# Optimization experiments

Hardware: AMD Instinct MI355X
Metric: run time of the kernel (lower is better)

The kernel has to match this reference:

```python
import jax, jax.numpy as jnp
import numpy as np

L = 4          # num_layers
H = 512        # hidden_size == input_size
B, S = 8, 4096
LN_EPS = 1e-5


def parallel_scan_log(coeffs, values):
    """h_t = coeffs_t * h_{t-1} + values_t via Hillis-Steele log-step scan.
    coeffs, values: (B, S, H). Faithful to the torch loop incl. clamp."""
    seq_len = coeffs.shape[1]
    a = jnp.clip(coeffs, 1e-08, 1.0 - 1e-08)
    b = values
    num_steps = int(seq_len - 1).bit_length()
    for step in range(num_steps):
        d = 1 << step
        if d >= seq_len:
            break
        a_prev = jnp.pad(a[:, :-d, :], ((0, 0), (d, 0), (0, 0)), constant_values=1.0)
        b_prev = jnp.pad(b[:, :-d, :], ((0, 0), (d, 0), (0, 0)), constant_values=0.0)
        b = a * b_prev + b   # uses old a (matches a_new/b_new then assign)
        a = a * a_prev
    return b


def mingru_layer(x, Wz, bz, Wh, bh):
    # x: (B,S,in) ; Wz,Wh: (H,in) torch Linear layout (y = x @ W.T + b)
    z = jax.nn.sigmoid(jnp.einsum('bsi,hi->bsh', x, Wz) + bz)
    h_tilde = jnp.tanh(jnp.einsum('bsi,hi->bsh', x, Wh) + bh)
    return parallel_scan_log(1.0 - z, z * h_tilde)


def layer_norm(x, g, b):
    mu = jnp.mean(x, axis=-1, keepdims=True)
    var = jnp.mean(jnp.square(x - mu), axis=-1, keepdims=True)
    return (x - mu) * jax.lax.rsqrt(var + LN_EPS) * g + b


def run_layers(x, Wz, bz, Wh, bh, ln_g, ln_b):
    h = x
    for i in range(L):
        h_new = mingru_layer(h, Wz[i], bz[i], Wh[i], bh[i])
        if i > 0:
            h_new = h_new + h  # residual (shapes match for i>0)
        h = layer_norm(h_new, ln_g, ln_b)  # dropout==Identity (p=0)
    return h


def setup_inputs() -> dict:
    key = jax.random.key(0)
    ks = jax.random.split(key, 12)
    lim = 1.0 / np.sqrt(H)  # torch Linear default init range
    u = lambda k, shp: jax.random.uniform(k, shp, jnp.float32, -lim, lim)
    return {
        'x': jax.random.normal(ks[0], (B, S, H), jnp.float32),
        'Wz_f': u(ks[1], (L, H, H)), 'bz_f': u(ks[2], (L, H)),
        'Wh_f': u(ks[3], (L, H, H)), 'bh_f': u(ks[4], (L, H)),
        'Wz_b': u(ks[5], (L, H, H)), 'bz_b': u(ks[6], (L, H)),
        'Wh_b': u(ks[7], (L, H, H)), 'bh_b': u(ks[8], (L, H)),
        'fusion_w': u(ks[9], (H, 2 * H)), 'fusion_b': u(ks[10], (H,)),
        'ln_g': jnp.ones((H,), jnp.float32), 'ln_b': jnp.zeros((H,), jnp.float32),
    }


def reference(x, Wz_f, bz_f, Wh_f, bh_f, Wz_b, bz_b, Wh_b, bh_b, fusion_w, fusion_b, ln_g, ln_b):
    out_fwd = run_layers(x, Wz_f, bz_f, Wh_f, bh_f, ln_g, ln_b)
    x_rev = jnp.flip(x, axis=1)
    out_bwd = jnp.flip(run_layers(x_rev, Wz_b, bz_b, Wh_b, bh_b, ln_g, ln_b), axis=1)
    out_comb = jnp.concatenate([out_fwd, out_bwd], axis=-1)  # (B,S,2H)
    return jnp.einsum('bsk,hk->bsh', out_comb, fusion_w) + fusion_b
```

## Files before the change

kernel.cpp:

```cpp
#include <hip/hip_runtime.h>

#define HID 512
#define SLEN 4096
#define NB 8
#define BSROWS (NB*SLEN)
#define NLAYER 4
#define CHUNKT 128
#define NCHUNK 32

typedef float f32x4 __attribute__((ext_vector_type(4)));
typedef unsigned int u32x4 __attribute__((ext_vector_type(4)));

typedef const __attribute__((address_space(1))) unsigned int* gas_u32p;
typedef __attribute__((address_space(3))) unsigned int* las_u32p;

__device__ __forceinline__ float bf2f(unsigned short u){
  union { unsigned int i; float f; } v; v.i = ((unsigned int)u) << 16; return v.f;
}
__device__ __forceinline__ unsigned short f2bf(float f){
  union { float f; unsigned int i; } v; v.f = f;
  unsigned int u = v.i;
  u = u + 0x7fffu + ((u >> 16) & 1u);
  return (unsigned short)(u >> 16);
}
__device__ __forceinline__ void mfma_bf16(f32x4& acc, u32x4 a, u32x4 b){
  asm("v_mfma_f32_16x16x32_bf16 %0, %1, %2, %0" : "+v"(acc) : "v"(a), "v"(b));
}
__device__ __forceinline__ void mfma_fence(){
  __builtin_amdgcn_sched_barrier(0);
  asm volatile("s_nop 7\n\ts_nop 7\n\ts_nop 7\n\ts_nop 7");
  __builtin_amdgcn_sched_barrier(0);
}
__device__ __forceinline__ void decode_ab(unsigned int v, float& a, float& b){
  a = (float)(v & 0xffffu) * (1.f/65535.f);
  b = fmaf((float)(v >> 16), 2.f/65535.f, -1.f);
}
__device__ __forceinline__ void gload_lds16(const unsigned short* g, unsigned short* l){
  __builtin_amdgcn_global_load_lds((gas_u32p)(const void*)g, (las_u32p)(void*)l, 16, 0, 0);
}
__device__ __forceinline__ int scidx(int row, int col){
  return row*64 + (col ^ (((row>>2)&3)<<4));
}


__global__ __launch_bounds__(256) void prep_w(
    const float* __restrict__ wzf, const float* __restrict__ whf,
    const float* __restrict__ wzb, const float* __restrict__ whb,
    unsigned short* __restrict__ wbf)
{
  int idx = blockIdx.x*256 + threadIdx.x;
  int i8  = idx & 63;
  int o   = (idx >> 6) & 511;
  int m   = (idx >> 15) & 1;
  int l   = (idx >> 16) & 3;
  int dir = idx >> 18;
  const float* src = dir ? (m ? whb : wzb) : (m ? whf : wzf);
  const float* p = src + ((size_t)(l*512 + o)*512 + i8*8);
  float4 v0 = *(const float4*)p;
  float4 v1 = *(const float4*)(p+4);
  unsigned short* q = wbf + ((((size_t)(dir*4 + l)*2 + m)*512 + o)*512 + i8*8);
  u32x4 outv;
  outv[0] = (unsigned)f2bf(v0.x) | ((unsigned)f2bf(v0.y)<<16);
  outv[1] = (unsigned)f2bf(v0.z) | ((unsigned)f2bf(v0.w)<<16);
  outv[2] = (unsigned)f2bf(v1.x) | ((unsigned)f2bf(v1.y)<<16);
  outv[3] = (unsigned)f2bf(v1.z) | ((unsigned)f2bf(v1.w)<<16);
  *(u32x4*)q = outv;
}

__global__ __launch_bounds__(256) void prep_fw(
    const float* __restrict__ fw, unsigned short* __restrict__ outw)
{
  int idx = blockIdx.x*256 + threadIdx.x;
  const float* p = fw + (size_t)idx*8;
  float4 v0 = *(const float4*)p;
  float4 v1 = *(const float4*)(p+4);
  u32x4 outv;
  outv[0] = (unsigned)f2bf(v0.x) | ((unsigned)f2bf(v0.y)<<16);
  outv[1] = (unsigned)f2bf(v0.z) | ((unsigned)f2bf(v0.w)<<16);
  outv[2] = (unsigned)f2bf(v1.x) | ((unsigned)f2bf(v1.y)<<16);
  outv[3] = (unsigned)f2bf(v1.z) | ((unsigned)f2bf(v1.w)<<16);
  *(u32x4*)(outw + (size_t)idx*8) = outv;
}

__global__ __launch_bounds__(256) void prep_x(
    const float* __restrict__ x, unsigned short* __restrict__ X0)
{
  int idx = blockIdx.x*256 + threadIdx.x;
  int j8  = idx & 63;
  int s   = (idx >> 6) & 4095;
  int b   = idx >> 18;
  const float* p = x + ((size_t)(b*SLEN + s)*512 + j8*8);
  float4 v0 = *(const float4*)p;
  float4 v1 = *(const float4*)(p+4);
  u32x4 outv;
  outv[0] = (unsigned)f2bf(v0.x) | ((unsigned)f2bf(v0.y)<<16);
  outv[1] = (unsigned)f2bf(v0.z) | ((unsigned)f2bf(v0.w)<<16);
  outv[2] = (unsigned)f2bf(v1.x) | ((unsigned)f2bf(v1.y)<<16);
  outv[3] = (unsigned)f2bf(v1.z) | ((unsigned)f2bf(v1.w)<<16);
  *(u32x4*)(X0 + ((size_t)(b*SLEN + s)*512 + j8*8)) = outv;
}


__global__ __launch_bounds__(256) void gate_gemm_scan(
    const unsigned short* __restrict__ X,
    const unsigned short* __restrict__ Wz,
    const unsigned short* __restrict__ Wh,
    const float* __restrict__ bzp, const float* __restrict__ bhp,
    unsigned int* __restrict__ PH,
    float* __restrict__ Aagg, float* __restrict__ Bagg,
    int Mtiles, int CG, int flip)
{
  __shared__ __align__(16) unsigned char smem[32768 + 2048];
  unsigned short* As  = (unsigned short*)smem;
  unsigned short* Bzs = (unsigned short*)(smem + 16384);
  unsigned short* Bhs = (unsigned short*)(smem + 24576);
  unsigned int*   SC  = (unsigned int*)smem;
  float* SegP = (float*)(smem + 32768);
  float* SegH = (float*)(smem + 32768 + 1024);

  int hw = blockIdx.x;
  int lg = (hw & 7)*Mtiles + (hw >> 3);
  int nt  = lg & 7;
  int mt  = lg >> 3;

  const int tid = threadIdx.x;
  const int lane = tid & 63;
  const int wv = tid >> 6;
  const int n0 = nt*64;
  const int slot = tid & 7;
  const int rowb = tid >> 3;

  f32x4 accz[2][4], acch[2][4];
  #pragma unroll
  for (int i=0;i<2;++i)
    #pragma unroll
    for (int j=0;j<4;++j){ accz[i][j] = (f32x4)(0.f); acch[i][j] = (f32x4)(0.f); }

  for (int ks=0; ks<8; ++ks){
    int k0 = ks*64;
    #pragma unroll
    for (int it=0; it<4; ++it){
      int row = rowb + it*32;
      int sr = (mt*128 + row) ^ flip;
      u32x4 v = *(const u32x4*)(X + (size_t)sr*512 + k0 + slot*8);
      *(u32x4*)(As + row*64 + ((slot ^ (row&7))<<3)) = v;
    }
    #pragma unroll
    for (int it=0; it<2; ++it){
      int row = rowb + it*32;
      u32x4 vz = *(const u32x4*)(Wz + (size_t)(n0+row)*512 + k0 + slot*8);
      *(u32x4*)(Bzs + row*64 + ((slot ^ (row&7))<<3)) = vz;
      u32x4 vh = *(const u32x4*)(Wh + (size_t)(n0+row)*512 + k0 + slot*8);
      *(u32x4*)(Bhs + row*64 + ((slot ^ (row&7))<<3)) = vh;
    }
    __syncthreads();
    #pragma unroll
    for (int kk=0; kk<2; ++kk){
      int kslot = kk*4 + (lane >> 4);
      u32x4 af[2];
      #pragma unroll
      for (int mf=0; mf<2; ++mf){
        int row = wv*32 + mf*16 + (lane & 15);
        af[mf] = *(const u32x4*)(As + row*64 + ((kslot ^ (row&7))<<3));
      }
      #pragma unroll
      for (int nf=0; nf<4; ++nf){
        int row = nf*16 + (lane & 15);
        u32x4 bz = *(const u32x4*)(Bzs + row*64 + ((kslot ^ (row&7))<<3));
        u32x4 bh = *(const u32x4*)(Bhs + row*64 + ((kslot ^ (row&7))<<3));
        #pragma unroll
        for (int mf=0; mf<2; ++mf){
          mfma_bf16(accz[mf][nf], af[mf], bz);
          mfma_bf16(acch[mf][nf], af[mf], bh);
        }
      }
    }
    __syncthreads();
  }
  mfma_fence();

  #pragma unroll
  for (int nf=0; nf<4; ++nf){
    int colL = nf*16 + (lane & 15);
    float bz = bzp[n0 + colL];
    float bh = bhp[n0 + colL];
    #pragma unroll
    for (int mf=0; mf<2; ++mf){
      int rloc = wv*32 + mf*16 + ((lane>>4)<<2);
      #pragma unroll
      for (int r=0; r<4; ++r){
        float zp = accz[mf][nf][r] + bz;
        float hp = acch[mf][nf][r] + bh;
        float sg = 1.f/(1.f + __expf(-zp));
        float th = 1.f - 2.f/(1.f + __expf(2.f*hp));
        float a = 1.f - sg;
        a = fminf(fmaxf(a, 1e-8f), 1.0f);
        float bv = sg*th;
        unsigned aq = (unsigned)fmaf(a, 65535.f, 0.5f);
        unsigned bq = (unsigned)fmaf(bv, 32767.5f, 32768.0f);
        SC[scidx(rloc + r, colL)] = aq | (bq << 16);
      }
    }
  }
  __syncthreads();

  const int col = tid & 63;
  const int seg = tid >> 6;
  {
    float P = 1.f, Hl = 0.f;
    #pragma unroll 8
    for (int r=0; r<32; ++r){
      float a, b; decode_ab(SC[scidx(seg*32 + r, col)], a, b);
      Hl = fmaf(a, Hl, b);
      P *= a;
    }
    SegP[seg*64 + col] = P;
    SegH[seg*64 + col] = Hl;
  }
  __syncthreads();

  float Ppre = 1.f, Hpre = 0.f;
  for (int j=0; j<seg; ++j){
    Hpre = fmaf(SegP[j*64 + col], Hpre, SegH[j*64 + col]);
    Ppre *= SegP[j*64 + col];
  }

  const int rowbase = mt*128;
  float pl = 1.f, hl = 0.f;
  float Pg = 1.f, Hg = 0.f;
  #pragma unroll 8
  for (int r=0; r<32; ++r){
    int row = seg*32 + r;
    float a, b; decode_ab(SC[scidx(row, col)], a, b);
    hl = fmaf(a, hl, b);
    pl *= a;
    Pg = Ppre * pl;
    Hg = fmaf(pl, Hpre, hl);
    unsigned pq = (unsigned)fmaf(Pg, 65535.f, 0.5f);
    PH[(size_t)(rowbase + row)*512 + n0 + col] = pq | ((unsigned)f2bf(Hg) << 16);
  }
  if (seg == 3){
    int chain = (mt >> 5)*512 + n0 + col;
    int c = mt & 31;
    Aagg[c*CG + chain] = Pg;
    Bagg[c*CG + chain] = Hg;
  }
}


__global__ __launch_bounds__(256) void scan_p2(
    const float* __restrict__ Aagg, const float* __restrict__ Bagg,
    float* __restrict__ Hin, int CG)
{
  int chain = blockIdx.x*256 + threadIdx.x;
  float hv = 0.f;
  #pragma unroll
  for (int c=0; c<NCHUNK; ++c){
    Hin[c*CG + chain] = hv;
    hv = fmaf(Aagg[c*CG + chain], hv, Bagg[c*CG + chain]);
  }
}


__global__ __launch_bounds__(256) void recon_ln(
    const unsigned int* __restrict__ PH,
    const float* __restrict__ Hin,
    unsigned short* __restrict__ Xio,
    const float* __restrict__ g, const float* __restrict__ bta,
    int resid, int CG)
{
  int token = blockIdx.x*4 + (threadIdx.x >> 6);
  int lane = threadIdx.x & 63;
  size_t base = (size_t)token*512 + lane*8;
  u32x4 p0 = *(const u32x4*)(PH + base);
  u32x4 p1 = *(const u32x4*)(PH + base + 4);
  int c  = (token >> 7) & 31;
  int bl = token >> 12;
  const float* hin = Hin + (size_t)c*CG + bl*512 + lane*8;
  f32x4 h0 = *(const f32x4*)hin;
  f32x4 h1 = *(const f32x4*)(hin + 4);
  float v[8];
  #pragma unroll
  for (int j=0; j<4; ++j){
    v[j]   = fmaf((float)(p0[j] & 0xffffu)*(1.f/65535.f), h0[j], bf2f((unsigned short)(p0[j] >> 16)));
    v[4+j] = fmaf((float)(p1[j] & 0xffffu)*(1.f/65535.f), h1[j], bf2f((unsigned short)(p1[j] >> 16)));
  }
  if (resid){
    u32x4 xv = *(const u32x4*)(Xio + base);
    #pragma unroll
    for (int w=0; w<4; ++w){
      v[2*w]   += bf2f((unsigned short)(xv[w] & 0xffffu));
      v[2*w+1] += bf2f((unsigned short)(xv[w] >> 16));
    }
  }
  float s = 0.f, s2 = 0.f;
  #pragma unroll
  for (int j=0; j<8; ++j){ s += v[j]; s2 += v[j]*v[j]; }
  #pragma unroll
  for (int o=1; o<64; o<<=1){ s += __shfl_xor(s, o, 64); s2 += __shfl_xor(s2, o, 64); }
  float mu = s * (1.f/512.f);
  float var = s2 * (1.f/512.f) - mu*mu;
  float inv = rsqrtf(var + 1e-5f);
  float4 g0 = *(const float4*)(g + lane*8);
  float4 g1 = *(const float4*)(g + lane*8 + 4);
  float4 b0 = *(const float4*)(bta + lane*8);
  float4 b1 = *(const float4*)(bta + lane*8 + 4);
  float gg[8]  = {g0.x,g0.y,g0.z,g0.w,g1.x,g1.y,g1.z,g1.w};
  float bbv[8] = {b0.x,b0.y,b0.z,b0.w,b1.x,b1.y,b1.z,b1.w};
  u32x4 outv;
  #pragma unroll
  for (int w=0; w<4; ++w){
    float y0 = (v[2*w]   - mu)*inv*gg[2*w]   + bbv[2*w];
    float y1 = (v[2*w+1] - mu)*inv*gg[2*w+1] + bbv[2*w+1];
    outv[w] = (unsigned)f2bf(y0) | ((unsigned)f2bf(y1) << 16);
  }
  *(u32x4*)(Xio + base) = outv;
}


__global__ __launch_bounds__(256) void fusion_gemm(
    const unsigned short* __restrict__ Xf,
    const unsigned short* __restrict__ Wf,
    const float* __restrict__ fb,
    float* __restrict__ outp)
{
  __shared__ __align__(16) unsigned short As[128*64];
  __shared__ __align__(16) unsigned short Bs[64*64];

  int hw = blockIdx.x;
  int lg = (hw & 7)*256 + (hw >> 3);
  int nt = lg & 7;
  int mt = lg >> 3;

  const int tid = threadIdx.x;
  const int lane = tid & 63;
  const int wv = tid >> 6;
  const int n0 = nt*64;
  const int lrow  = lane >> 3;
  const int slotp = (lane & 7) ^ (lrow & 7);

  f32x4 acc[2][4];
  #pragma unroll
  for (int i=0;i<2;++i)
    #pragma unroll
    for (int j=0;j<4;++j) acc[i][j] = (f32x4)(0.f);

  for (int ks=0; ks<16; ++ks){
    int k0 = ks*64;
    const unsigned short* Abase = Xf + ((k0 >= 512) ? (size_t)BSROWS*512 : 0);
    int kc = k0 & 511;
    int flip = (k0 >= 512) ? 4095 : 0;
    #pragma unroll
    for (int it=0; it<4; ++it){
      int row = it*32 + wv*8 + lrow;
      int sr = (mt*128 + row) ^ flip;
      gload_lds16(Abase + (size_t)sr*512 + kc + slotp*8,
                  As + (it*32 + wv*8)*64);
    }
    #pragma unroll
    for (int it=0; it<2; ++it){
      int row = it*32 + wv*8 + lrow;
      gload_lds16(Wf + (size_t)(n0 + row)*1024 + k0 + slotp*8,
                  Bs + (it*32 + wv*8)*64);
    }
    __syncthreads();
    #pragma unroll
    for (int kk=0; kk<2; ++kk){
      int kslot = kk*4 + (lane >> 4);
      u32x4 af[2];
      #pragma unroll
      for (int mf=0; mf<2; ++mf){
        int row = wv*32 + mf*16 + (lane & 15);
        af[mf] = *(const u32x4*)(As + row*64 + ((kslot ^ (row&7))<<3));
      }
      #pragma unroll
      for (int nf=0; nf<4; ++nf){
        int row = nf*16 + (lane & 15);
        u32x4 bv = *(const u32x4*)(Bs + row*64 + ((kslot ^ (row&7))<<3));
        #pragma unroll
        for (int mf=0; mf<2; ++mf) mfma_bf16(acc[mf][nf], af[mf], bv);
      }
    }
    __syncthreads();
  }
  mfma_fence();

  #pragma unroll
  for (int nf=0; nf<4; ++nf){
    int col = n0 + nf*16 + (lane & 15);
    float bias = fb[col];
    #pragma unroll
    for (int mf=0; mf<2; ++mf){
      int rb = mt*128 + wv*32 + mf*16 + ((lane>>4)<<2);
      #pragma unroll
      for (int r=0; r<4; ++r)
        outp[(size_t)(rb + r)*512 + col] = acc[mf][nf][r] + bias;
    }
  }
}


extern "C" void kernel_launch(void* const* d_in, const int* in_sizes, int n_in,
                              void* d_out, int out_size, void* d_ws, size_t ws_size,
                              hipStream_t stream)
{
  (void)in_sizes; (void)n_in; (void)out_size;
  const float* x   = (const float*)d_in[0];
  const float* wzf = (const float*)d_in[1];
  const float* bzf = (const float*)d_in[2];
  const float* whf = (const float*)d_in[3];
  const float* bhf = (const float*)d_in[4];
  const float* wzb = (const float*)d_in[5];
  const float* bzb = (const float*)d_in[6];
  const float* whb = (const float*)d_in[7];
  const float* bhb = (const float*)d_in[8];
  const float* fw  = (const float*)d_in[9];
  const float* fbb = (const float*)d_in[10];
  const float* lng = (const float*)d_in[11];
  const float* lnb = (const float*)d_in[12];
  float* outp = (float*)d_out;

  const size_t WbfB = (size_t)16*512*512*2;
  const size_t WfbB = (size_t)512*1024*2;
  const size_t XB   = (size_t)2*BSROWS*512*2;
  const size_t aggB = (size_t)4096*NCHUNK*4;
  int SG = 8;
  for (int c = 1; c <= 8; c <<= 1){
    size_t need = WbfB + WfbB + XB + 3*aggB
                + ((size_t)BSROWS/c)*512*4
                + 1024;
    if (need <= ws_size){ SG = c; break; }
  }
  const int R  = BSROWS / SG;
  const int NBg = NB / SG;
  const int CG = NBg * 512;
  const int Mtiles = R / 128;

  char* ws = (char*)d_ws;
  size_t o = 0;
  unsigned short* Wbf = (unsigned short*)(ws + o); o += WbfB;
  unsigned short* Wfb = (unsigned short*)(ws + o); o += WfbB;
  unsigned short* X   = (unsigned short*)(ws + o); o += XB;
  unsigned int*   PH  = (unsigned int*)  (ws + o); o += (size_t)R*512*4;
  float* Aagg = (float*)(ws + o); o += aggB;
  float* Bagg = (float*)(ws + o); o += aggB;
  float* Hin  = (float*)(ws + o); o += aggB;

  prep_w <<<2048, 256, 0, stream>>>(wzf, whf, wzb, whb, Wbf);
  prep_fw<<<256,  256, 0, stream>>>(fw, Wfb);
  prep_x <<<8192, 256, 0, stream>>>(x, X);

  #define CHAIN(Xin_, Xg_, WzP_, WhP_, bzP_, bhP_, flip_, resid_)            \
    do {                                                                     \
      gate_gemm_scan<<<Mtiles*8, 256, 0, stream>>>(Xin_, WzP_, WhP_,         \
          bzP_, bhP_, PH, Aagg, Bagg, Mtiles, CG, flip_);                    \
      scan_p2 <<<CG/256, 256, 0, stream>>>(Aagg, Bagg, Hin, CG);             \
      recon_ln<<<R/4,    256, 0, stream>>>(PH, Hin, Xg_, lng, lnb, resid_, CG); \
    } while (0)

  for (int g = 0; g < SG; ++g){
    unsigned short* X0g = X + (size_t)g*R*512;
    unsigned short* X1g = X + ((size_t)BSROWS + (size_t)g*R)*512;
    const unsigned short* Wz = Wbf + ((size_t)((1*4 + 0)*2 + 0))*(512*512);
    const unsigned short* Wh = Wbf + ((size_t)((1*4 + 0)*2 + 1))*(512*512);
    CHAIN(X0g, X1g, Wz, Wh, bzb + 0*512, bhb + 0*512, 4095, 0);
  }
  for (int g = 0; g < SG; ++g){
    unsigned short* X0g = X + (size_t)g*R*512;
    for (int l = 0; l < NLAYER; ++l){
      const unsigned short* Wz = Wbf + ((size_t)((0*4 + l)*2 + 0))*(512*512);
      const unsigned short* Wh = Wbf + ((size_t)((0*4 + l)*2 + 1))*(512*512);
      CHAIN(X0g, X0g, Wz, Wh, bzf + l*512, bhf + l*512, 0, l > 0 ? 1 : 0);
    }
  }
  for (int g = 0; g < SG; ++g){
    unsigned short* X1g = X + ((size_t)BSROWS + (size_t)g*R)*512;
    for (int l = 1; l < NLAYER; ++l){
      const unsigned short* Wz = Wbf + ((size_t)((1*4 + l)*2 + 0))*(512*512);
      const unsigned short* Wh = Wbf + ((size_t)((1*4 + l)*2 + 1))*(512*512);
      CHAIN(X1g, X1g, Wz, Wh, bzb + l*512, bhb + l*512, 0, 1);
    }
  }
  #undef CHAIN

  fusion_gemm<<<2048, 256, 0, stream>>>(X, Wfb, fbb, outp);
}
```

Before: 700.8 us.

## Batch forward and backward directions into single per-layer launches

Each gate GEMM/scan, chunk-scan and recon/LayerNorm launch now covers both directions and all batch rows for a layer. This replaces the per-group, per-direction launch sequence. The second direction's intermediate PH buffer lives in the output buffer, so the code no longer sizes groups from the workspace. The aim is fewer launches and larger grids with better occupancy. The cost is a larger workspace requirement and reliance on d_out as scratch before the final GEMM.

```diff
diff --git a/kernel.cpp b/kernel.cpp
--- a/kernel.cpp
+++ b/kernel.cpp
@@ -7,6 +7,8 @@
 #define NLAYER 4
 #define CHUNKT 128
 #define NCHUNK 32
+#define MTPD 256
+#define CGALL 8192
 
 typedef float f32x4 __attribute__((ext_vector_type(4)));
 typedef unsigned int u32x4 __attribute__((ext_vector_type(4)));
@@ -103,12 +105,13 @@
 
 __global__ __launch_bounds__(256) void gate_gemm_scan(
     const unsigned short* __restrict__ X,
-    const unsigned short* __restrict__ Wz,
-    const unsigned short* __restrict__ Wh,
-    const float* __restrict__ bzp, const float* __restrict__ bhp,
-    unsigned int* __restrict__ PH,
+    const unsigned short* __restrict__ Wbf,
+    const float* __restrict__ bzf, const float* __restrict__ bhf,
+    const float* __restrict__ bzb, const float* __restrict__ bhb,
+    unsigned int* __restrict__ PH0,
+    unsigned int* __restrict__ PH1,
     float* __restrict__ Aagg, float* __restrict__ Bagg,
-    int Mtiles, int CG, int flip)
+    int layer, int xoff1, int flip1)
 {
   __shared__ __align__(16) unsigned char smem[32768 + 2048];
   unsigned short* As  = (unsigned short*)smem;
@@ -119,9 +122,19 @@
   float* SegH = (float*)(smem + 32768 + 1024);
 
   int hw = blockIdx.x;
-  int lg = (hw & 7)*Mtiles + (hw >> 3);
+  int dir = hw >= (MTPD*8);
+  int hwl = hw - dir*(MTPD*8);
+  int lg = (hwl & 7)*MTPD + (hwl >> 3);
   int nt  = lg & 7;
   int mt  = lg >> 3;
+
+  const unsigned short* Xp = X + (size_t)(dir ? xoff1 : 0)*512;
+  const int flip = dir ? flip1 : 0;
+  const unsigned short* Wz = Wbf + ((size_t)((dir*4 + layer)*2 + 0))*(512*512);
+  const unsigned short* Wh = Wbf + ((size_t)((dir*4 + layer)*2 + 1))*(512*512);
+  const float* bzp = (dir ? bzb : bzf) + layer*512;
+  const float* bhp = (dir ? bhb : bhf) + layer*512;
+  unsigned int* PHp = dir ? PH1 : PH0;
 
   const int tid = threadIdx.x;
   const int lane = tid & 63;
@@ -142,7 +155,7 @@
     for (int it=0; it<4; ++it){
       int row = rowb + it*32;
       int sr = (mt*128 + row) ^ flip;
-      u32x4 v = *(const u32x4*)(X + (size_t)sr*512 + k0 + slot*8);
+      u32x4 v = *(const u32x4*)(Xp + (size_t)sr*512 + k0 + slot*8);
       *(u32x4*)(As + row*64 + ((slot ^ (row&7))<<3)) = v;
     }
     #pragma unroll
@@ -237,46 +250,48 @@
     Pg = Ppre * pl;
     Hg = fmaf(pl, Hpre, hl);
     unsigned pq = (unsigned)fmaf(Pg, 65535.f, 0.5f);
-    PH[(size_t)(rowbase + row)*512 + n0 + col] = pq | ((unsigned)f2bf(Hg) << 16);
+    PHp[(size_t)(rowbase + row)*512 + n0 + col] = pq | ((unsigned)f2bf(Hg) << 16);
   }
   if (seg == 3){
-    int chain = (mt >> 5)*512 + n0 + col;
+    int chain = dir*4096 + (mt >> 5)*512 + n0 + col;
     int c = mt & 31;
-    Aagg[c*CG + chain] = Pg;
-    Bagg[c*CG + chain] = Hg;
+    Aagg[c*CGALL + chain] = Pg;
+    Bagg[c*CGALL + chain] = Hg;
   }
 }
 
 
 __global__ __launch_bounds__(256) void scan_p2(
     const float* __restrict__ Aagg, const float* __restrict__ Bagg,
-    float* __restrict__ Hin, int CG)
+    float* __restrict__ Hin)
 {
   int chain = blockIdx.x*256 + threadIdx.x;
   float hv = 0.f;
   #pragma unroll
   for (int c=0; c<NCHUNK; ++c){
-    Hin[c*CG + chain] = hv;
-    hv = fmaf(Aagg[c*CG + chain], hv, Bagg[c*CG + chain]);
+    Hin[c*CGALL + chain] = hv;
+    hv = fmaf(Aagg[c*CGALL + chain], hv, Bagg[c*CGALL + chain]);
   }
 }
 
 
 __global__ __launch_bounds__(256) void recon_ln(
-    const unsigned int* __restrict__ PH,
+    const unsigned int* __restrict__ PH0,
+    const unsigned int* __restrict__ PH1,
     const float* __restrict__ Hin,
     unsigned short* __restrict__ Xio,
-    const float* __restrict__ g, const float* __restrict__ bta,
-    int resid, int CG)
+    const float* __restrict__ g, const float* __restrict__ bta, int resid)
 {
   int token = blockIdx.x*4 + (threadIdx.x >> 6);
   int lane = threadIdx.x & 63;
-  size_t base = (size_t)token*512 + lane*8;
-  u32x4 p0 = *(const u32x4*)(PH + base);
-  u32x4 p1 = *(const u32x4*)(PH + base + 4);
-  int c  = (token >> 7) & 31;
-  int bl = token >> 12;
-  const float* hin = Hin + (size_t)c*CG + bl*512 + lane*8;
+  int dir  = token >> 15;
+  int tloc = token & (BSROWS-1);
+  const unsigned int* PHp = dir ? PH1 : PH0;
+  size_t pbase = (size_t)tloc*512 + lane*8;
+  u32x4 p0 = *(const u32x4*)(PHp + pbase);
+  u32x4 p1 = *(const u32x4*)(PHp + pbase + 4);
+  int c = (tloc >> 7) & 31;
+  const float* hin = Hin + (size_t)c*CGALL + (token >> 12)*512 + lane*8;
   f32x4 h0 = *(const f32x4*)hin;
   f32x4 h1 = *(const f32x4*)(hin + 4);
   float v[8];
@@ -285,6 +300,7 @@
     v[j]   = fmaf((float)(p0[j] & 0xffffu)*(1.f/65535.f), h0[j], bf2f((unsigned short)(p0[j] >> 16)));
     v[4+j] = fmaf((float)(p1[j] & 0xffffu)*(1.f/65535.f), h1[j], bf2f((unsigned short)(p1[j] >> 16)));
   }
+  size_t base = (size_t)token*512 + lane*8;
   if (resid){
     u32x4 xv = *(const u32x4*)(Xio + base);
     #pragma unroll
@@ -404,7 +420,7 @@
                               void* d_out, int out_size, void* d_ws, size_t ws_size,
                               hipStream_t stream)
 {
-  (void)in_sizes; (void)n_in; (void)out_size;
+  (void)in_sizes; (void)n_in; (void)out_size; (void)ws_size;
   const float* x   = (const float*)d_in[0];
   const float* wzf = (const float*)d_in[1];
   const float* bzf = (const float*)d_in[2];
@@ -420,68 +436,29 @@
   const float* lnb = (const float*)d_in[12];
   float* outp = (float*)d_out;
 
-  const size_t WbfB = (size_t)16*512*512*2;
-  const size_t WfbB = (size_t)512*1024*2;
-  const size_t XB   = (size_t)2*BSROWS*512*2;
-  const size_t aggB = (size_t)4096*NCHUNK*4;
-  int SG = 8;
-  for (int c = 1; c <= 8; c <<= 1){
-    size_t need = WbfB + WfbB + XB + 3*aggB
-                + ((size_t)BSROWS/c)*512*4
-                + 1024;
-    if (need <= ws_size){ SG = c; break; }
-  }
-  const int R  = BSROWS / SG;
-  const int NBg = NB / SG;
-  const int CG = NBg * 512;
-  const int Mtiles = R / 128;
-
   char* ws = (char*)d_ws;
   size_t o = 0;
-  unsigned short* Wbf = (unsigned short*)(ws + o); o += WbfB;
-  unsigned short* Wfb = (unsigned short*)(ws + o); o += WfbB;
-  unsigned short* X   = (unsigned short*)(ws + o); o += XB;
-  unsigned int*   PH  = (unsigned int*)  (ws + o); o += (size_t)R*512*4;
-  float* Aagg = (float*)(ws + o); o += aggB;
-  float* Bagg = (float*)(ws + o); o += aggB;
-  float* Hin  = (float*)(ws + o); o += aggB;
+  unsigned short* Wbf = (unsigned short*)(ws + o); o += (size_t)16*512*512*2;
+  unsigned short* Wfb = (unsigned short*)(ws + o); o += (size_t)512*1024*2;
+  unsigned short* X   = (unsigned short*)(ws + o); o += (size_t)2*BSROWS*512*2;
+  unsigned int*   PH0 = (unsigned int*)  (ws + o); o += (size_t)BSROWS*512*4;
+  float* Aagg = (float*)(ws + o); o += (size_t)CGALL*NCHUNK*4;
+  float* Bagg = (float*)(ws + o); o += (size_t)CGALL*NCHUNK*4;
+  float* Hin  = (float*)(ws + o); o += (size_t)CGALL*NCHUNK*4;
+  unsigned int* PH1 = (unsigned int*)d_out;
 
   prep_w <<<2048, 256, 0, stream>>>(wzf, whf, wzb, whb, Wbf);
   prep_fw<<<256,  256, 0, stream>>>(fw, Wfb);
   prep_x <<<8192, 256, 0, stream>>>(x, X);
 
-  #define CHAIN(Xin_, Xg_, WzP_, WhP_, bzP_, bhP_, flip_, resid_)            \
-    do {                                                                     \
-      gate_gemm_scan<<<Mtiles*8, 256, 0, stream>>>(Xin_, WzP_, WhP_,         \
-          bzP_, bhP_, PH, Aagg, Bagg, Mtiles, CG, flip_);                    \
-      scan_p2 <<<CG/256, 256, 0, stream>>>(Aagg, Bagg, Hin, CG);             \
-      recon_ln<<<R/4,    256, 0, stream>>>(PH, Hin, Xg_, lng, lnb, resid_, CG); \
-    } while (0)
-
-  for (int g = 0; g < SG; ++g){
-    unsigned short* X0g = X + (size_t)g*R*512;
-    unsigned short* X1g = X + ((size_t)BSROWS + (size_t)g*R)*512;
-    const unsigned short* Wz = Wbf + ((size_t)((1*4 + 0)*2 + 0))*(512*512);
-    const unsigned short* Wh = Wbf + ((size_t)((1*4 + 0)*2 + 1))*(512*512);
-    CHAIN(X0g, X1g, Wz, Wh, bzb + 0*512, bhb + 0*512, 4095, 0);
-  }
-  for (int g = 0; g < SG; ++g){
-    unsigned short* X0g = X + (size_t)g*R*512;
-    for (int l = 0; l < NLAYER; ++l){
-      const unsigned short* Wz = Wbf + ((size_t)((0*4 + l)*2 + 0))*(512*512);
-      const unsigned short* Wh = Wbf + ((size_t)((0*4 + l)*2 + 1))*(512*512);
-      CHAIN(X0g, X0g, Wz, Wh, bzf + l*512, bhf + l*512, 0, l > 0 ? 1 : 0);
-    }
-  }
-  for (int g = 0; g < SG; ++g){
-    unsigned short* X1g = X + ((size_t)BSROWS + (size_t)g*R)*512;
-    for (int l = 1; l < NLAYER; ++l){
-      const unsigned short* Wz = Wbf + ((size_t)((1*4 + l)*2 + 0))*(512*512);
-      const unsigned short* Wh = Wbf + ((size_t)((1*4 + l)*2 + 1))*(512*512);
-      CHAIN(X1g, X1g, Wz, Wh, bzb + l*512, bhb + l*512, 0, 1);
-    }
-  }
-  #undef CHAIN
+  for (int l = 0; l < NLAYER; ++l){
+    int xoff1 = (l == 0) ? 0 : BSROWS;
+    int flip1 = (l == 0) ? 4095 : 0;
+    gate_gemm_scan<<<4096, 256, 0, stream>>>(X, Wbf, bzf, bhf, bzb, bhb,
+                                             PH0, PH1, Aagg, Bagg, l, xoff1, flip1);
+    scan_p2 <<<CGALL/256, 256, 0, stream>>>(Aagg, Bagg, Hin);
+    recon_ln<<<16384, 256, 0, stream>>>(PH0, PH1, Hin, X, lng, lnb, l > 0 ? 1 : 0);
+  }
 
   fusion_gemm<<<2048, 256, 0, stream>>>(X, Wfb, fbb, outp);
 }
```

Measured after the change: 665.2 us. 5.1% less time.
